# Performance work log

Hardware: AMD Instinct MI355X
Metric: run time of the kernel (lower is better)

The kernel has to match this reference:

```python
import jax, jax.numpy as jnp
import numpy as np

EMBED_DIM = 1024
NUM_HEADS = 16
HEAD_DIM = EMBED_DIM // NUM_HEADS
SCALE = HEAD_DIM ** -0.5


def setup_inputs() -> dict:
    key = jax.random.key(0)
    k_x, k_wqkv, k_bqkv, k_wo, k_bo = jax.random.split(key, 5)
    B, T, C = 2, 2048, EMBED_DIM
    bound = 1.0 / np.sqrt(C)
    return {
        "x": jax.random.normal(k_x, (B, T, C), dtype=jnp.float32),
        "w_qkv": jax.random.uniform(k_wqkv, (C, 3 * C), jnp.float32, -bound, bound),
        "b_qkv": jax.random.uniform(k_bqkv, (3 * C,), jnp.float32, -bound, bound),
        "w_out": jax.random.uniform(k_wo, (C, C), jnp.float32, -bound, bound),
        "b_out": jax.random.uniform(k_bo, (C,), jnp.float32, -bound, bound),
    }


def reference(x, w_qkv, b_qkv, w_out, b_out):
    B, T, C = x.shape
    H, D = NUM_HEADS, HEAD_DIM
    qkv = x @ w_qkv + b_qkv                      # [B,T,3C]
    q, k, v = jnp.split(qkv, 3, axis=-1)         # each [B,T,C]
    q = q.reshape(B, T, H, D).transpose(0, 2, 1, 3)  # [B,H,T,D]
    k = k.reshape(B, T, H, D).transpose(0, 2, 1, 3)
    v = v.reshape(B, T, H, D).transpose(0, 2, 1, 3)
    scores = jnp.einsum("bhqd,bhkd->bhqk", q, k) * SCALE  # [B,H,T,T]
    weights = jax.nn.softmax(scores, axis=-1)
    out = jnp.einsum("bhqk,bhkd->bhqd", weights, v)       # [B,H,T,D]
    concat = out.transpose(0, 2, 1, 3).reshape(B, T, C)
    return concat @ w_out + b_out
```

## Files before the change

kernel.cpp:

```cpp
#include <hip/hip_runtime.h>

typedef _Float16 f16;
typedef _Float16 f16x8 __attribute__((ext_vector_type(8)));
typedef _Float16 f16x4 __attribute__((ext_vector_type(4)));
typedef float f32x4 __attribute__((ext_vector_type(4)));
typedef float f32x16 __attribute__((ext_vector_type(16)));
typedef unsigned int u32x4 __attribute__((ext_vector_type(4)));

#define SCALE_Q (0.125f * 1.44269504088896f)

__device__ __forceinline__ f32x4 mfma16x16x32(f16x8 a, f16x8 b, f32x4 c) {
  return __builtin_amdgcn_mfma_f32_16x16x32_f16(a, b, c, 0, 0, 0);
}
__device__ __forceinline__ f32x16 mfma32x32x16(f16x8 a, f16x8 b, f32x16 c) {
  return __builtin_amdgcn_mfma_f32_32x32x16_f16(a, b, c, 0, 0, 0);
}

__device__ __forceinline__ float fexp2(float x) {
  float r;
  asm("v_exp_f32 %0, %1" : "=v"(r) : "v"(x));
  return r;
}

typedef const __attribute__((address_space(1))) void* gptr1;
typedef __attribute__((address_space(3))) void* lptr3;
__device__ __forceinline__ void gload_lds16(const void* g, void* l) {
  __builtin_amdgcn_global_load_lds((gptr1)g, (lptr3)l, 16, 0, 0);
}

__device__ __forceinline__ unsigned pk2(float a, float b) {
  return __builtin_bit_cast(unsigned, __builtin_amdgcn_cvt_pkrtz(a, b));
}

__global__ __launch_bounds__(256)
void cvt_f32_f16(const float* __restrict__ in, f16* __restrict__ out, int n4) {
  int i = blockIdx.x * 256 + threadIdx.x;
  if (i >= n4) return;
  float4 v = reinterpret_cast<const float4*>(in)[i];
  f16x4 o = {(f16)v.x, (f16)v.y, (f16)v.z, (f16)v.w};
  reinterpret_cast<f16x4*>(out)[i] = o;
}

__global__ __launch_bounds__(256)
void transpose_cvt(const float* __restrict__ in, f16* __restrict__ out, int R, int Cin) {
  __shared__ float tile[32][33];
  int bx = blockIdx.x * 32;
  int by = blockIdx.y * 32;
  int tx = threadIdx.x & 31, ty = threadIdx.x >> 5;
#pragma unroll
  for (int i = ty; i < 32; i += 8)
    tile[i][tx] = in[(size_t)(by + i) * Cin + bx + tx];
  __syncthreads();
#pragma unroll
  for (int i = ty; i < 32; i += 8)
    out[(size_t)(bx + i) * R + by + tx] = (f16)tile[tx][i];
}

__global__ __launch_bounds__(256)
void gemm_qkv(const f16* __restrict__ A, const f16* __restrict__ Bt,
              const float* __restrict__ bias, f16* __restrict__ qQ,
              f16* __restrict__ kP, f16* __restrict__ vP) {
  constexpr int BM = 128, BN = 128, BK = 32, K = 1024, N = 3072;
  __shared__ f16 As[BM * BK];
  __shared__ f16 Bs[BN * BK];
  const int tid = threadIdx.x;
  const int l = tid & 63;
  const int w = tid >> 6;
  const int wr = w >> 1, wc = w & 1;
  const int bm = blockIdx.x * BM, bn = blockIdx.y * BN;
  const int l15 = l & 15, lhi = l >> 4;

  f32x4 acc[4][4] = {};

  const char* Ab = (const char*)A;
  const char* Bb = (const char*)Bt;
  const size_t rowbytes = (size_t)K * 2;

  for (int kt = 0; kt < K; kt += BK) {
    __syncthreads();
#pragma unroll
    for (int c = 0; c < 2; ++c) {
      int o = tid * 16 + c * 4096;
      int r = o >> 6;
      int cb = o & 63;
      gload_lds16(Ab + (size_t)(bm + r) * rowbytes + (size_t)kt * 2 + cb, (char*)As + o);
      gload_lds16(Bb + (size_t)(bn + r) * rowbytes + (size_t)kt * 2 + cb, (char*)Bs + o);
    }
    __syncthreads();

    f16x8 af[4], bf[4];
#pragma unroll
    for (int i = 0; i < 4; ++i)
      af[i] = *reinterpret_cast<const f16x8*>(&As[(wr * 64 + i * 16 + l15) * BK + 8 * lhi]);
#pragma unroll
    for (int i = 0; i < 4; ++i)
      bf[i] = *reinterpret_cast<const f16x8*>(&Bs[(wc * 64 + i * 16 + l15) * BK + 8 * lhi]);
#pragma unroll
    for (int i = 0; i < 4; ++i)
#pragma unroll
      for (int j = 0; j < 4; ++j)
        acc[i][j] = mfma16x16x32(af[i], bf[j], acc[i][j]);
  }

  const int region = bn >> 10;
#pragma unroll
  for (int i = 0; i < 4; ++i) {
#pragma unroll
    for (int j = 0; j < 4; ++j) {
      int gr0 = bm + wr * 64 + i * 16 + 4 * lhi;
      int gc = bn + wc * 64 + j * 16 + l15;
      float bia = bias[gc];
      if (region == 0) {
#pragma unroll
        for (int r = 0; r < 4; ++r) {
          float v = (acc[i][j][r] + bia) * SCALE_Q;
          qQ[(size_t)(gr0 + r) * 1024 + gc] = (f16)v;
        }
      } else if (region == 1) {
        int dloc = gc - 1024;
        int h = dloc >> 6, dd = dloc & 63;
        int kd = dd >> 4, hi8 = (dd >> 3) & 1, j8 = dd & 7;
        int bb = gr0 >> 11;
        int pair = bb * 16 + h;
#pragma unroll
        for (int r = 0; r < 4; ++r) {
          int key = (gr0 + r) & 2047;
          int t32 = key >> 5, l31k = key & 31;
          size_t idx = ((((size_t)pair * 64 + t32) * 4 + kd) * 64 + (hi8 * 32 + l31k)) * 8 + j8;
          kP[idx] = (f16)(acc[i][j][r] + bia);
        }
      } else {
        int dloc = gc - 2048;
        int h = dloc >> 6, dd = dloc & 63;
        int dhalf = dd >> 5, l31v = dd & 31;
        int bb = gr0 >> 11;
        int pair = bb * 16 + h;
        int key = gr0 & 2047;
        int t64 = key >> 6;
        int k6 = key & 63;
        int ks = k6 >> 4, hiv = (k6 >> 3) & 1, jv = k6 & 7;
        int rr = dhalf * 4 + ks;
        size_t idx = ((((size_t)pair * 32 + t64) * 8 + rr) * 64 + (hiv * 32 + l31v)) * 8 + jv;
        f16x4 ov;
#pragma unroll
        for (int r = 0; r < 4; ++r) ov[r] = (f16)(acc[i][j][r] + bia);
        *reinterpret_cast<f16x4*>(&vP[idx]) = ov;
      }
    }
  }
}

__global__ __launch_bounds__(256)
void gemm_out(const f16* __restrict__ A, const f16* __restrict__ Bt,
              const float* __restrict__ bias, float* __restrict__ outf,
              int M, int N, int K) {
  constexpr int BM = 128, BN = 128, BK = 32;
  __shared__ f16 As[BM * BK];
  __shared__ f16 Bs[BN * BK];
  const int tid = threadIdx.x;
  const int l = tid & 63;
  const int w = tid >> 6;
  const int wr = w >> 1, wc = w & 1;
  const int bm = blockIdx.x * BM, bn = blockIdx.y * BN;
  const int l15 = l & 15, lhi = l >> 4;

  f32x4 acc[4][4] = {};

  const char* Ab = (const char*)A;
  const char* Bb = (const char*)Bt;
  const size_t rowbytes = (size_t)K * 2;

  for (int kt = 0; kt < K; kt += BK) {
    __syncthreads();
#pragma unroll
    for (int c = 0; c < 2; ++c) {
      int o = tid * 16 + c * 4096;
      int r = o >> 6;
      int cb = o & 63;
      gload_lds16(Ab + (size_t)(bm + r) * rowbytes + (size_t)kt * 2 + cb, (char*)As + o);
      gload_lds16(Bb + (size_t)(bn + r) * rowbytes + (size_t)kt * 2 + cb, (char*)Bs + o);
    }
    __syncthreads();

    f16x8 af[4], bf[4];
#pragma unroll
    for (int i = 0; i < 4; ++i)
      af[i] = *reinterpret_cast<const f16x8*>(&As[(wr * 64 + i * 16 + l15) * BK + 8 * lhi]);
#pragma unroll
    for (int i = 0; i < 4; ++i)
      bf[i] = *reinterpret_cast<const f16x8*>(&Bs[(wc * 64 + i * 16 + l15) * BK + 8 * lhi]);
#pragma unroll
    for (int i = 0; i < 4; ++i)
#pragma unroll
      for (int j = 0; j < 4; ++j)
        acc[i][j] = mfma16x16x32(af[i], bf[j], acc[i][j]);
  }

#pragma unroll
  for (int i = 0; i < 4; ++i) {
#pragma unroll
    for (int j = 0; j < 4; ++j) {
      int gr0 = bm + wr * 64 + i * 16 + 4 * lhi;
      int gc = bn + wc * 64 + j * 16 + l15;
      float b = bias[gc];
#pragma unroll
      for (int r = 0; r < 4; ++r)
        outf[(size_t)(gr0 + r) * N + gc] = acc[i][j][r] + b;
    }
  }
}

__global__ __launch_bounds__(256, 3)
void attn_kernel(const f16* __restrict__ qQ, const f16* __restrict__ kP,
                 const f16* __restrict__ vP, f16* __restrict__ outh) {
  constexpr int T = 2048;
  __shared__ float mo[4096];
  __shared__ float MlBuf[2][64];

  const int tid = threadIdx.x;
  const int l = tid & 63;
  const int w = tid >> 6;
  const int wq = w >> 1;
  const int grp = w & 1;
  const int l31 = l & 31, hi = l >> 5;

  const int bid = blockIdx.x;
  const int pair = bid & 31;
  const int b = pair >> 4;
  const int h = pair & 15;
  const int qt = bid >> 5;

  const int q0 = qt * 64 + wq * 32;

  f16x8 bq[4];
  {
    const f16* qp = qQ + (size_t)(b * T + q0 + l31) * 1024 + h * 64 + hi * 8;
#pragma unroll
    for (int kd = 0; kd < 4; ++kd)
      bq[kd] = *reinterpret_cast<const f16x8*>(qp + kd * 16);
  }

  const f16* Kp = kP + (size_t)pair * 131072;
  const f16* Vp = vP + (size_t)pair * 131072;

  f32x16 o0 = {}, o1 = {};
  float l_r = 0.f;

  for (int t = 0; t < 16; ++t) {
    const int t64g = grp * 16 + t;
    const int t32g = t64g * 2;

    f16x8 ak[2][4];
#pragma unroll
    for (int kt = 0; kt < 2; ++kt)
#pragma unroll
      for (int kd = 0; kd < 4; ++kd)
        ak[kt][kd] = *reinterpret_cast<const f16x8*>(
            Kp + ((((size_t)t32g + kt) * 4 + kd) * 64 + l) * 8);

    f16x8 av0[4], av1[4];
#pragma unroll
    for (int ks = 0; ks < 4; ++ks) {
      av0[ks] = *reinterpret_cast<const f16x8*>(
          Vp + (((size_t)t64g * 8 + ks) * 64 + l) * 8);
      av1[ks] = *reinterpret_cast<const f16x8*>(
          Vp + (((size_t)t64g * 8 + 4 + ks) * 64 + l) * 8);
    }

    f32x16 s0 = {}, s1 = {};
    __builtin_amdgcn_s_setprio(1);
#pragma unroll
    for (int kd = 0; kd < 4; ++kd) s0 = mfma32x32x16(ak[0][kd], bq[kd], s0);
#pragma unroll
    for (int kd = 0; kd < 4; ++kd) s1 = mfma32x32x16(ak[1][kd], bq[kd], s1);
    __builtin_amdgcn_s_setprio(0);

    float sm[16];
#pragma unroll
    for (int r = 0; r < 16; ++r) {
      s0[r] = fexp2(s0[r]);
      s1[r] = fexp2(s1[r]);
      sm[r] = s0[r] + s1[r];
    }
#pragma unroll
    for (int st = 8; st > 0; st >>= 1)
#pragma unroll
      for (int r = 0; r < st; ++r) sm[r] += sm[r + st];
    l_r += sm[0] + __shfl_xor(sm[0], 32);

    f16x8 bp[4];
#pragma unroll
    for (int kt = 0; kt < 2; ++kt) {
#pragma unroll
      for (int s2 = 0; s2 < 2; ++s2) {
        u32x4 wd;
#pragma unroll
        for (int u = 0; u < 2; ++u) {
          float a0 = kt ? s1[8 * s2 + 2 * u] : s0[8 * s2 + 2 * u];
          float a1 = kt ? s1[8 * s2 + 2 * u + 1] : s0[8 * s2 + 2 * u + 1];
          float b0 = kt ? s1[8 * s2 + 4 + 2 * u] : s0[8 * s2 + 4 + 2 * u];
          float b1 = kt ? s1[8 * s2 + 4 + 2 * u + 1] : s0[8 * s2 + 4 + 2 * u + 1];
          unsigned wB = pk2(a0, a1);
          unsigned wA = pk2(b0, b1);
          unsigned oB = __shfl_xor(wB, 32);
          unsigned oA = __shfl_xor(wA, 32);
          wd[u]     = hi ? oA : wB;
          wd[2 + u] = hi ? wA : oB;
        }
        bp[2 * kt + s2] = __builtin_bit_cast(f16x8, wd);
      }
    }

    __builtin_amdgcn_s_setprio(1);
#pragma unroll
    for (int ks = 0; ks < 4; ++ks) {
      o0 = mfma32x32x16(av0[ks], bp[ks], o0);
      o1 = mfma32x32x16(av1[ks], bp[ks], o1);
    }
    __builtin_amdgcn_s_setprio(0);
  }

  const int mbase = wq * 2048 + l * 32;
  if (grp == 1) {
#pragma unroll
    for (int k = 0; k < 8; ++k) {
      int ks = k ^ (l & 7);
      f32x4 v;
      if (k < 4) { v = f32x4{o0[4*k], o0[4*k+1], o0[4*k+2], o0[4*k+3]}; }
      else       { int r = 4*(k-4); v = f32x4{o1[r], o1[r+1], o1[r+2], o1[r+3]}; }
      *reinterpret_cast<f32x4*>(&mo[mbase + ks * 4]) = v;
    }
    MlBuf[wq][l] = l_r;
  }
  __syncthreads();
  if (grp == 0) {
    float inv = 1.0f / (l_r + MlBuf[wq][l]);
    f16* orow = outh + (size_t)(b * T + q0 + l31) * 1024 + h * 64;
#pragma unroll
    for (int k = 0; k < 8; ++k) {
      int ks = k ^ (l & 7);
      f32x4 ob = *reinterpret_cast<const f32x4*>(&mo[mbase + ks * 4]);
#pragma unroll
      for (int j = 0; j < 4; ++j) {
        int r = 4 * (k & 3) + j;
        int d = (r & 3) + 8 * (r >> 2) + 4 * hi;
        float own = (k < 4) ? o0[r] : o1[r];
        float val = (own + ob[j]) * inv;
        orow[(k < 4 ? d : d + 32)] = (f16)val;
      }
    }
  }
}

extern "C" void kernel_launch(void* const* d_in, const int* in_sizes, int n_in,
                              void* d_out, int out_size, void* d_ws, size_t ws_size,
                              hipStream_t stream) {
  const float* x      = (const float*)d_in[0];
  const float* w_qkv  = (const float*)d_in[1];
  const float* b_qkv  = (const float*)d_in[2];
  const float* w_out  = (const float*)d_in[3];
  const float* b_out  = (const float*)d_in[4];
  float* out = (float*)d_out;

  char* ws = (char*)d_ws;
  f16* xh    = (f16*)(ws);
  f16* wqkvT = (f16*)(ws + 8388608);
  f16* qQ    = (f16*)(ws + 16777216);
  f16* kP    = (f16*)(ws + 25165824);
  f16* vP    = (f16*)(ws + 33554432);
  f16* attnh = (f16*)(ws + 41943040);
  f16* woutT = (f16*)(ws);

  cvt_f32_f16<<<4096, 256, 0, stream>>>(x, xh, 1048576);
  transpose_cvt<<<dim3(96, 32), 256, 0, stream>>>(w_qkv, wqkvT, 1024, 3072);
  gemm_qkv<<<dim3(32, 24), 256, 0, stream>>>(xh, wqkvT, b_qkv, qQ, kP, vP);
  transpose_cvt<<<dim3(32, 32), 256, 0, stream>>>(w_out, woutT, 1024, 1024);
  attn_kernel<<<1024, 256, 0, stream>>>(qQ, kP, vP, attnh);
  gemm_out<<<dim3(32, 8), 256, 0, stream>>>(attnh, woutT, b_out, out, 4096, 1024, 1024);
}
```

Measured before the change: 131.8 us.

## Split K/V fragment loads to cut register pressure and raise occupancy to 4 waves

The attention kernel's launch bound goes from 3 to 4 blocks per CU. To fit that register budget, the K fragments are loaded in two halves that reuse one register array, and the second V half is loaded only after the softmax, so fewer values are live at once. The inline-asm v_exp_f32 is replaced with the compiler builtin, which gives the scheduler more freedom. The trade-off is less load latency hiding inside each wave and serialized loads, and forcing the tighter register cap could cause spills.

```diff
diff --git a/kernel.cpp b/kernel.cpp
--- a/kernel.cpp
+++ b/kernel.cpp
@@ -17,9 +17,7 @@
 }
 
 __device__ __forceinline__ float fexp2(float x) {
-  float r;
-  asm("v_exp_f32 %0, %1" : "=v"(r) : "v"(x));
-  return r;
+  return __builtin_amdgcn_exp2f(x);
 }
 
 typedef const __attribute__((address_space(1))) void* gptr1;
@@ -210,7 +208,7 @@
   }
 }
 
-__global__ __launch_bounds__(256, 3)
+__global__ __launch_bounds__(256, 4)
 void attn_kernel(const f16* __restrict__ qQ, const f16* __restrict__ kP,
                  const f16* __restrict__ vP, f16* __restrict__ outh) {
   constexpr int T = 2048;
@@ -250,30 +248,32 @@
     const int t64g = grp * 16 + t;
     const int t32g = t64g * 2;
 
-    f16x8 ak[2][4];
-#pragma unroll
-    for (int kt = 0; kt < 2; ++kt)
-#pragma unroll
-      for (int kd = 0; kd < 4; ++kd)
-        ak[kt][kd] = *reinterpret_cast<const f16x8*>(
-            Kp + ((((size_t)t32g + kt) * 4 + kd) * 64 + l) * 8);
-
-    f16x8 av0[4], av1[4];
-#pragma unroll
-    for (int ks = 0; ks < 4; ++ks) {
+    f16x8 ak[4];
+#pragma unroll
+    for (int kd = 0; kd < 4; ++kd)
+      ak[kd] = *reinterpret_cast<const f16x8*>(
+          Kp + (((size_t)t32g * 4 + kd) * 64 + l) * 8);
+    f32x16 s0 = {};
+    __builtin_amdgcn_s_setprio(1);
+#pragma unroll
+    for (int kd = 0; kd < 4; ++kd) s0 = mfma32x32x16(ak[kd], bq[kd], s0);
+    __builtin_amdgcn_s_setprio(0);
+
+#pragma unroll
+    for (int kd = 0; kd < 4; ++kd)
+      ak[kd] = *reinterpret_cast<const f16x8*>(
+          Kp + ((((size_t)t32g + 1) * 4 + kd) * 64 + l) * 8);
+    f32x16 s1 = {};
+    __builtin_amdgcn_s_setprio(1);
+#pragma unroll
+    for (int kd = 0; kd < 4; ++kd) s1 = mfma32x32x16(ak[kd], bq[kd], s1);
+    __builtin_amdgcn_s_setprio(0);
+
+    f16x8 av0[4];
+#pragma unroll
+    for (int ks = 0; ks < 4; ++ks)
       av0[ks] = *reinterpret_cast<const f16x8*>(
           Vp + (((size_t)t64g * 8 + ks) * 64 + l) * 8);
-      av1[ks] = *reinterpret_cast<const f16x8*>(
-          Vp + (((size_t)t64g * 8 + 4 + ks) * 64 + l) * 8);
-    }
-
-    f32x16 s0 = {}, s1 = {};
-    __builtin_amdgcn_s_setprio(1);
-#pragma unroll
-    for (int kd = 0; kd < 4; ++kd) s0 = mfma32x32x16(ak[0][kd], bq[kd], s0);
-#pragma unroll
-    for (int kd = 0; kd < 4; ++kd) s1 = mfma32x32x16(ak[1][kd], bq[kd], s1);
-    __builtin_amdgcn_s_setprio(0);
 
     float sm[16];
 #pragma unroll
@@ -311,12 +311,17 @@
       }
     }
 
+    f16x8 av1[4];
+#pragma unroll
+    for (int ks = 0; ks < 4; ++ks)
+      av1[ks] = *reinterpret_cast<const f16x8*>(
+          Vp + (((size_t)t64g * 8 + 4 + ks) * 64 + l) * 8);
+
     __builtin_amdgcn_s_setprio(1);
 #pragma unroll
-    for (int ks = 0; ks < 4; ++ks) {
-      o0 = mfma32x32x16(av0[ks], bp[ks], o0);
-      o1 = mfma32x32x16(av1[ks], bp[ks], o1);
-    }
+    for (int ks = 0; ks < 4; ++ks) o0 = mfma32x32x16(av0[ks], bp[ks], o0);
+#pragma unroll
+    for (int ks = 0; ks < 4; ++ks) o1 = mfma32x32x16(av1[ks], bp[ks], o1);
     __builtin_amdgcn_s_setprio(0);
   }
 
```

After: 140.2 us. 1.06x slower.

## Fuse prep kernels into one launch and remap GEMM blocks per XCD

Applied to the files above, without the earlier changes.

Merges the x conversion and both weight transpose-convert kernels into a single prep launch. The w_out transpose moves to its own workspace region so it can run before the QKV GEMM. Both GEMMs switch to a 1D grid with an XCD-aware block-to-tile mapping, so blocks on the same XCD share A/B tiles in L2. This cuts two kernel launches and aims to improve cache locality, at the cost of some index arithmetic and hardcoded shapes in gemm_out. It also swaps the inline-asm exp for the builtin.

```diff
diff --git a/kernel.cpp b/kernel.cpp
--- a/kernel.cpp
+++ b/kernel.cpp
@@ -17,9 +17,7 @@
 }
 
 __device__ __forceinline__ float fexp2(float x) {
-  float r;
-  asm("v_exp_f32 %0, %1" : "=v"(r) : "v"(x));
-  return r;
+  return __builtin_amdgcn_exp2f(x);
 }
 
 typedef const __attribute__((address_space(1))) void* gptr1;
@@ -33,20 +31,32 @@
 }
 
 __global__ __launch_bounds__(256)
-void cvt_f32_f16(const float* __restrict__ in, f16* __restrict__ out, int n4) {
-  int i = blockIdx.x * 256 + threadIdx.x;
-  if (i >= n4) return;
-  float4 v = reinterpret_cast<const float4*>(in)[i];
-  f16x4 o = {(f16)v.x, (f16)v.y, (f16)v.z, (f16)v.w};
-  reinterpret_cast<f16x4*>(out)[i] = o;
-}
-
-__global__ __launch_bounds__(256)
-void transpose_cvt(const float* __restrict__ in, f16* __restrict__ out, int R, int Cin) {
+void prep(const float* __restrict__ x, f16* __restrict__ xh,
+          const float* __restrict__ w_qkv, f16* __restrict__ wqkvT,
+          const float* __restrict__ w_out, f16* __restrict__ woutT) {
   __shared__ float tile[32][33];
-  int bx = blockIdx.x * 32;
-  int by = blockIdx.y * 32;
-  int tx = threadIdx.x & 31, ty = threadIdx.x >> 5;
+  const int bid = blockIdx.x;
+  const int tid = threadIdx.x;
+  if (bid < 4096) {
+    int i = bid * 256 + tid;
+    float4 v = reinterpret_cast<const float4*>(x)[i];
+    f16x4 o = {(f16)v.x, (f16)v.y, (f16)v.z, (f16)v.w};
+    reinterpret_cast<f16x4*>(xh)[i] = o;
+    return;
+  }
+  const float* in;
+  f16* out;
+  int bx, by, R, Cin;
+  if (bid < 7168) {
+    int t = bid - 4096;
+    in = w_qkv; out = wqkvT; R = 1024; Cin = 3072;
+    bx = (t % 96) * 32; by = (t / 96) * 32;
+  } else {
+    int t = bid - 7168;
+    in = w_out; out = woutT; R = 1024; Cin = 1024;
+    bx = (t % 32) * 32; by = (t / 32) * 32;
+  }
+  int tx = tid & 31, ty = tid >> 5;
 #pragma unroll
   for (int i = ty; i < 32; i += 8)
     tile[i][tx] = in[(size_t)(by + i) * Cin + bx + tx];
@@ -60,14 +70,19 @@
 void gemm_qkv(const f16* __restrict__ A, const f16* __restrict__ Bt,
               const float* __restrict__ bias, f16* __restrict__ qQ,
               f16* __restrict__ kP, f16* __restrict__ vP) {
-  constexpr int BM = 128, BN = 128, BK = 32, K = 1024, N = 3072;
+  constexpr int BM = 128, BN = 128, BK = 32, K = 1024;
   __shared__ f16 As[BM * BK];
   __shared__ f16 Bs[BN * BK];
   const int tid = threadIdx.x;
   const int l = tid & 63;
   const int w = tid >> 6;
   const int wr = w >> 1, wc = w & 1;
-  const int bm = blockIdx.x * BM, bn = blockIdx.y * BN;
+  const int bid = blockIdx.x;
+  const int xcd = bid & 7, idx = bid >> 3;
+  const int xg = xcd & 3, yg = xcd >> 2;
+  const int mx = xg * 8 + (idx & 7);
+  const int ny = yg * 12 + (idx >> 3);
+  const int bm = mx * BM, bn = ny * BN;
   const int l15 = l & 15, lhi = l >> 4;
 
   f32x4 acc[4][4] = {};
@@ -126,8 +141,8 @@
         for (int r = 0; r < 4; ++r) {
           int key = (gr0 + r) & 2047;
           int t32 = key >> 5, l31k = key & 31;
-          size_t idx = ((((size_t)pair * 64 + t32) * 4 + kd) * 64 + (hi8 * 32 + l31k)) * 8 + j8;
-          kP[idx] = (f16)(acc[i][j][r] + bia);
+          size_t idxp = ((((size_t)pair * 64 + t32) * 4 + kd) * 64 + (hi8 * 32 + l31k)) * 8 + j8;
+          kP[idxp] = (f16)(acc[i][j][r] + bia);
         }
       } else {
         int dloc = gc - 2048;
@@ -140,11 +155,11 @@
         int k6 = key & 63;
         int ks = k6 >> 4, hiv = (k6 >> 3) & 1, jv = k6 & 7;
         int rr = dhalf * 4 + ks;
-        size_t idx = ((((size_t)pair * 32 + t64) * 8 + rr) * 64 + (hiv * 32 + l31v)) * 8 + jv;
+        size_t idxp = ((((size_t)pair * 32 + t64) * 8 + rr) * 64 + (hiv * 32 + l31v)) * 8 + jv;
         f16x4 ov;
 #pragma unroll
         for (int r = 0; r < 4; ++r) ov[r] = (f16)(acc[i][j][r] + bia);
-        *reinterpret_cast<f16x4*>(&vP[idx]) = ov;
+        *reinterpret_cast<f16x4*>(&vP[idxp]) = ov;
       }
     }
   }
@@ -152,16 +167,19 @@
 
 __global__ __launch_bounds__(256)
 void gemm_out(const f16* __restrict__ A, const f16* __restrict__ Bt,
-              const float* __restrict__ bias, float* __restrict__ outf,
-              int M, int N, int K) {
-  constexpr int BM = 128, BN = 128, BK = 32;
+              const float* __restrict__ bias, float* __restrict__ outf) {
+  constexpr int BM = 128, BN = 128, BK = 32, K = 1024, N = 1024;
   __shared__ f16 As[BM * BK];
   __shared__ f16 Bs[BN * BK];
   const int tid = threadIdx.x;
   const int l = tid & 63;
   const int w = tid >> 6;
   const int wr = w >> 1, wc = w & 1;
-  const int bm = blockIdx.x * BM, bn = blockIdx.y * BN;
+  const int bid = blockIdx.x;
+  const int xcd = bid & 7, idx = bid >> 3;
+  const int mx = xcd * 4 + (idx & 3);
+  const int ny = idx >> 2;
+  const int bm = mx * BM, bn = ny * BN;
   const int l15 = l & 15, lhi = l >> 4;
 
   f32x4 acc[4][4] = {};
@@ -365,16 +383,14 @@
   char* ws = (char*)d_ws;
   f16* xh    = (f16*)(ws);
   f16* wqkvT = (f16*)(ws + 8388608);
+  f16* woutT = (f16*)(ws + 14680064);
   f16* qQ    = (f16*)(ws + 16777216);
   f16* kP    = (f16*)(ws + 25165824);
   f16* vP    = (f16*)(ws + 33554432);
   f16* attnh = (f16*)(ws + 41943040);
-  f16* woutT = (f16*)(ws);
-
-  cvt_f32_f16<<<4096, 256, 0, stream>>>(x, xh, 1048576);
-  transpose_cvt<<<dim3(96, 32), 256, 0, stream>>>(w_qkv, wqkvT, 1024, 3072);
-  gemm_qkv<<<dim3(32, 24), 256, 0, stream>>>(xh, wqkvT, b_qkv, qQ, kP, vP);
-  transpose_cvt<<<dim3(32, 32), 256, 0, stream>>>(w_out, woutT, 1024, 1024);
+
+  prep<<<8192, 256, 0, stream>>>(x, xh, w_qkv, wqkvT, w_out, woutT);
+  gemm_qkv<<<768, 256, 0, stream>>>(xh, wqkvT, b_qkv, qQ, kP, vP);
   attn_kernel<<<1024, 256, 0, stream>>>(qQ, kP, vP, attnh);
-  gemm_out<<<dim3(32, 8), 256, 0, stream>>>(attnh, woutT, b_out, out, 4096, 1024, 1024);
-}
+  gemm_out<<<256, 256, 0, stream>>>(attnh, woutT, b_out, out);
+}
```

Result: faster. 125.0 us (-5.2%).
